# Kernel optimization log

Hardware: AMD Instinct MI355X
Metric: run time of the kernel (lower is better)

The kernel has to match this reference:

```python
import jax, jax.numpy as jnp
import numpy as np

TEMPERATURE = 0.07
EPS = 1e-8  # torch CosineSimilarity eps


def setup_inputs() -> dict:
    key = jax.random.key(0)
    k1, k2, k3 = jax.random.split(key, 3)
    N, D = 8192, 512
    features = jax.random.normal(k1, (N, D), dtype=jnp.float32)
    positive_mask = jax.random.randint(k2, (N, N), 0, 2, dtype=jnp.int32)
    negative_mask = jax.random.randint(k3, (N, N), 0, 2, dtype=jnp.int32)
    return {"features": features, "positive_mask": positive_mask, "negative_mask": negative_mask}


def reference(features, positive_mask, negative_mask):
    N = positive_mask.shape[0]
    self_contrast = 1.0 - jnp.eye(N, dtype=features.dtype)  # zero diagonal
    pos = positive_mask.astype(features.dtype) * self_contrast  # [N, N]
    neg = negative_mask.astype(features.dtype) * self_contrast  # [N, N]

    # cosine similarity via normalized matmul (same math as broadcasted CosineSimilarity)
    norm = jnp.maximum(jnp.linalg.norm(features, axis=1, keepdims=True), EPS)
    fn = features / norm  # [N, D]
    sim = jnp.matmul(fn, fn.T) / TEMPERATURE  # [N, N]

    logits_max = jax.lax.stop_gradient(jnp.max(sim, axis=1, keepdims=True))
    e = jnp.exp(sim - logits_max)  # [N, N]

    positives = e * pos
    log_neg_sum = jnp.log(jnp.sum(e * neg, axis=1, keepdims=True))  # [N, 1]
    log_prob = positives - log_neg_sum  # [N, N] (faithful to source: exp-masked, not log)

    cardinal = jnp.sum(pos, axis=1)
    cardinal = jnp.where(cardinal == 0, 1.0, cardinal)
    log_prob_sum = jnp.sum(log_prob * pos, axis=1)
    loss = -log_prob_sum / cardinal
    return jnp.mean(loss)
```

## Files before the change

### kernel.cpp

```cpp
#include <hip/hip_runtime.h>
#include <hip/hip_bf16.h>
#include <math.h>

#define NN 8192
#define DD 512
#define INV_T 14.285714285714286f

typedef __attribute__((ext_vector_type(8))) short s16x8;
typedef __attribute__((ext_vector_type(4))) float f32x4;
typedef __attribute__((ext_vector_type(4))) int   i32x4;
typedef __attribute__((ext_vector_type(4))) unsigned int u32x4;

__device__ __forceinline__ unsigned short f32_to_bf16(float f) {
  unsigned int u = __float_as_uint(f);
  u += 0x7FFFu + ((u >> 16) & 1u);
  return (unsigned short)(u >> 16);
}

__global__ __launch_bounds__(256) void normalize_kernel(const float* __restrict__ f,
                                                        unsigned short* __restrict__ fnb) {
  const int wave = threadIdx.x >> 6;
  const int lane = threadIdx.x & 63;
  const int row  = blockIdx.x * 4 + wave;
  const float* src = f + (size_t)row * DD + lane * 8;
  float4 v0 = *(const float4*)src;
  float4 v1 = *(const float4*)(src + 4);
  float ss = v0.x*v0.x + v0.y*v0.y + v0.z*v0.z + v0.w*v0.w
           + v1.x*v1.x + v1.y*v1.y + v1.z*v1.z + v1.w*v1.w;
  #pragma unroll
  for (int o = 32; o; o >>= 1) ss += __shfl_xor(ss, o);
  const float r = 1.0f / fmaxf(sqrtf(ss), 1e-8f);
  ushort4 a, b;
  a.x = f32_to_bf16(v0.x * r); a.y = f32_to_bf16(v0.y * r);
  a.z = f32_to_bf16(v0.z * r); a.w = f32_to_bf16(v0.w * r);
  b.x = f32_to_bf16(v1.x * r); b.y = f32_to_bf16(v1.y * r);
  b.z = f32_to_bf16(v1.z * r); b.w = f32_to_bf16(v1.w * r);
  unsigned short* dst = fnb + (size_t)row * DD + lane * 8;
  *(ushort4*)dst = a;
  *(ushort4*)(dst + 4) = b;
}

__global__ __launch_bounds__(256, 3) void fused_kernel(const unsigned short* __restrict__ fnb,
                                                       const int* __restrict__ posm,
                                                       const int* __restrict__ negm,
                                                       float* __restrict__ Spos,
                                                       float* __restrict__ Sneg,
                                                       float* __restrict__ Pcnt) {
  const int bid = blockIdx.x;
  int bi = (int)(64.5 - sqrt(64.5 * 64.5 - 2.0 * (double)bid));
  while (64 * bi - bi * (bi - 1) / 2 > bid) --bi;
  while (64 * (bi + 1) - (bi + 1) * bi / 2 <= bid) ++bi;
  const int bj = bi + (bid - (64 * bi - bi * (bi - 1) / 2));
  const int I = bi * 128;
  const int J = bj * 128;
  const bool offdiag = (bi != bj);

  const int tid  = threadIdx.x;
  const int wave = tid >> 6;
  const int lane = tid & 63;
  const int wm = wave >> 1;
  const int wn = wave & 1;
  const int q   = lane >> 4;
  const int c16 = lane & 15;

  __shared__ unsigned int bdir[2][128][4];
  __shared__ unsigned int btr [2][128][4];

  {
    const int tile = wave >> 1;
    const int msel = wave & 1;
    const int R0 = tile ? J : I;
    const int C0 = tile ? I : J;
    const int* mb = msel ? negm : posm;
    unsigned int (*dst)[4] = tile ? btr[msel] : bdir[msel];
    const int sub  = lane >> 5;
    const int col4 = (lane & 31) * 4;
    if (!(tile && !offdiag)) {
      for (int i = 0; i < 64; i += 4) {
        i32x4 v[4];
        #pragma unroll
        for (int u = 0; u < 4; ++u) {
          const int row = (i + u) * 2 + sub;
          v[u] = __builtin_nontemporal_load(
                   (const i32x4*)(mb + (size_t)(R0 + row) * NN + C0 + col4));
        }
        #pragma unroll
        for (int u = 0; u < 4; ++u) {
          const unsigned long long b0 = __ballot(v[u].x != 0);
          const unsigned long long b1 = __ballot(v[u].y != 0);
          const unsigned long long b2 = __ballot(v[u].z != 0);
          const unsigned long long b3 = __ballot(v[u].w != 0);
          if (lane < 2) {
            const int sh = lane * 32;
            u32x4 w;
            w.x = (unsigned int)(b0 >> sh);
            w.y = (unsigned int)(b1 >> sh);
            w.z = (unsigned int)(b2 >> sh);
            w.w = (unsigned int)(b3 >> sh);
            *(u32x4*)&dst[(i + u) * 2 + lane][0] = w;
          }
        }
      }
    }
  }

  f32x4 acc[4][4];
  const f32x4 z4 = {0.f, 0.f, 0.f, 0.f};
  #pragma unroll
  for (int mt = 0; mt < 4; ++mt)
    #pragma unroll
    for (int nt = 0; nt < 4; ++nt) acc[mt][nt] = z4;

  const unsigned short* aP[4];
  const unsigned short* bP[4];
  #pragma unroll
  for (int t = 0; t < 4; ++t) {
    aP[t] = fnb + (size_t)(I + wm * 64 + t * 16 + c16) * DD + q * 8;
    bP[t] = fnb + (size_t)(J + wn * 64 + t * 16 + c16) * DD + q * 8;
  }
  s16x8 aF[2][4], bF[2][4];
  #pragma unroll
  for (int t = 0; t < 4; ++t) {
    aF[0][t] = *(const s16x8*)aP[t];
    bF[0][t] = *(const s16x8*)bP[t];
  }
  #pragma unroll 2
  for (int kk = 0; kk < DD / 32; ++kk) {
    const int cur = kk & 1, nxt = cur ^ 1;
    if (kk < DD / 32 - 1) {
      const int off = (kk + 1) * 32;
      #pragma unroll
      for (int t = 0; t < 4; ++t) {
        aF[nxt][t] = *(const s16x8*)(aP[t] + off);
        bF[nxt][t] = *(const s16x8*)(bP[t] + off);
      }
    }
    #pragma unroll
    for (int mt = 0; mt < 4; ++mt)
      #pragma unroll
      for (int nt = 0; nt < 4; ++nt)
        acc[mt][nt] = __builtin_amdgcn_mfma_f32_16x16x32_bf16(aF[cur][mt], bF[cur][nt], acc[mt][nt], 0, 0, 0);
  }

  __syncthreads();

  const bool hasdiag = (bi == bj) && (wm == wn);

  u32x4 pT4[4], nT4[4];
  if (offdiag) {
    #pragma unroll
    for (int nt = 0; nt < 4; ++nt) {
      const int cl = wn * 64 + nt * 16 + c16;
      pT4[nt] = *(const u32x4*)&btr[0][cl][0];
      nT4[nt] = *(const u32x4*)&btr[1][cl][0];
    }
  }
  float tsp[4] = {0,0,0,0}, tsn[4] = {0,0,0,0};
  const int jword = c16 & 3;
  const int cshift = c16 >> 2;

  #pragma unroll
  for (int mt = 0; mt < 4; ++mt) {
    const int rl = wm * 64 + mt * 16 + q * 4;
    unsigned int pwv[4], nwv[4];
    #pragma unroll
    for (int r = 0; r < 4; ++r) {
      pwv[r] = bdir[0][rl + r][jword];
      nwv[r] = bdir[1][rl + r][jword];
    }
    float dsp[4] = {0,0,0,0}, dsn[4] = {0,0,0,0}, dpc[4] = {0,0,0,0};
    #pragma unroll
    for (int nt = 0; nt < 4; ++nt) {
      float e[4];
      #pragma unroll
      for (int r = 0; r < 4; ++r)
        e[r] = __expf(acc[mt][nt][r] * INV_T - INV_T);
      const int cbit = wn * 16 + nt * 4 + cshift;
      const int cl   = wn * 64 + nt * 16 + c16;
      #pragma unroll
      for (int r = 0; r < 4; ++r) {
        float pf = (float)((pwv[r] >> cbit) & 1u);
        float nf = (float)((nwv[r] >> cbit) & 1u);
        if (hasdiag && (rl + r == cl)) { pf = 0.f; nf = 0.f; }
        dsp[r] = fmaf(e[r], pf, dsp[r]);
        dsn[r] = fmaf(e[r], nf, dsn[r]);
        dpc[r] += pf;
      }
      if (offdiag) {
        const int tc = wm * 16 + mt * 4 + q;
        const unsigned int* pw = (const unsigned int*)&pT4[nt];
        const unsigned int* nw = (const unsigned int*)&nT4[nt];
        #pragma unroll
        for (int r = 0; r < 4; ++r) {
          tsp[nt] = fmaf(e[r], (float)((pw[r] >> tc) & 1u), tsp[nt]);
          tsn[nt] = fmaf(e[r], (float)((nw[r] >> tc) & 1u), tsn[nt]);
        }
      }
    }
    #pragma unroll
    for (int r = 0; r < 4; ++r) {
      float a = dsp[r], b = dsn[r], p = dpc[r];
      #pragma unroll
      for (int o = 1; o <= 8; o <<= 1) {
        a += __shfl_xor(a, o);
        b += __shfl_xor(b, o);
        p += __shfl_xor(p, o);
      }
      if (c16 == 0) {
        const int row = I + rl + r;
        atomicAdd(&Spos[row], a);
        atomicAdd(&Sneg[row], b);
        atomicAdd(&Pcnt[row], p);
      }
    }
  }

  if (offdiag) {
    #pragma unroll
    for (int nt = 0; nt < 4; ++nt) {
      float a = tsp[nt], b = tsn[nt];
      a += __shfl_xor(a, 16); a += __shfl_xor(a, 32);
      b += __shfl_xor(b, 16); b += __shfl_xor(b, 32);
      const int col = J + wn * 64 + nt * 16 + c16;
      if (q == 0) {
        atomicAdd(&Spos[col], a);
        atomicAdd(&Sneg[col], b);
      }
      if (q == 0 && wm == 0) {
        const unsigned int* pw = (const unsigned int*)&pT4[nt];
        const float pc = (float)(__popc(pw[0]) + __popc(pw[1]) + __popc(pw[2]) + __popc(pw[3]));
        atomicAdd(&Pcnt[col], pc);
      }
    }
  }
}

__global__ __launch_bounds__(256) void finalize_kernel(const float* __restrict__ Spos,
                                                       const float* __restrict__ Sneg,
                                                       const float* __restrict__ Pcnt,
                                                       float* __restrict__ out) {
  float local = 0.f;
  for (int i = threadIdx.x; i < NN; i += 256) {
    const float sp = Spos[i], sn = Sneg[i], pc = Pcnt[i];
    const float card = (pc == 0.f) ? 1.f : pc;
    local += (logf(sn) * pc - sp) / card;
  }
  #pragma unroll
  for (int o = 32; o; o >>= 1) local += __shfl_xor(local, o);
  __shared__ float red[4];
  if ((threadIdx.x & 63) == 0) red[threadIdx.x >> 6] = local;
  __syncthreads();
  if (threadIdx.x == 0)
    out[0] = (red[0] + red[1] + red[2] + red[3]) * (1.0f / (float)NN);
}

extern "C" void kernel_launch(void* const* d_in, const int* in_sizes, int n_in,
                              void* d_out, int out_size, void* d_ws, size_t ws_size,
                              hipStream_t stream) {
  const float* feat = (const float*)d_in[0];
  const int* posm   = (const int*)d_in[1];
  const int* negm   = (const int*)d_in[2];
  float* out = (float*)d_out;

  char* ws = (char*)d_ws;
  unsigned short* fnb = (unsigned short*)ws;
  float* Spos = (float*)(ws + (size_t)8 * 1024 * 1024);
  float* Sneg = Spos + NN;
  float* Pcnt = Sneg + NN;

  hipMemsetAsync(Spos, 0, 3 * NN * sizeof(float), stream);
  normalize_kernel<<<NN / 4, 256, 0, stream>>>(feat, fnb);
  fused_kernel<<<2080, 256, 0, stream>>>(fnb, posm, negm, Spos, Sneg, Pcnt);
  finalize_kernel<<<1, 256, 0, stream>>>(Spos, Sneg, Pcnt, out);
}
```

Before: 658.3 us.

## Interleave mask streaming with MFMA k-loop via software-pipelined loads

Mask loads and bit-packing no longer run as a separate phase before the matmul. They are split into 16 groups and issued three groups ahead inside the fully unrolled k-loop, so their HBM latency overlaps with the MFMA work. The bf16 fragment double buffer is dropped in favour of loading operands each iteration, and the occupancy hint drops from 3 to 2 waves per SIMD to make room for the mask register buffers. The risks are higher register pressure, lower occupancy and weaker latency hiding for the feature loads.

```diff
diff --git a/kernel.cpp b/kernel.cpp
--- a/kernel.cpp
+++ b/kernel.cpp
@@ -40,7 +40,7 @@
   *(ushort4*)(dst + 4) = b;
 }
 
-__global__ __launch_bounds__(256, 3) void fused_kernel(const unsigned short* __restrict__ fnb,
+__global__ __launch_bounds__(256, 2) void fused_kernel(const unsigned short* __restrict__ fnb,
                                                        const int* __restrict__ posm,
                                                        const int* __restrict__ negm,
                                                        float* __restrict__ Spos,
@@ -66,43 +66,47 @@
   __shared__ unsigned int bdir[2][128][4];
   __shared__ unsigned int btr [2][128][4];
 
-  {
-    const int tile = wave >> 1;
-    const int msel = wave & 1;
-    const int R0 = tile ? J : I;
-    const int C0 = tile ? I : J;
-    const int* mb = msel ? negm : posm;
-    unsigned int (*dst)[4] = tile ? btr[msel] : bdir[msel];
-    const int sub  = lane >> 5;
-    const int col4 = (lane & 31) * 4;
-    if (!(tile && !offdiag)) {
-      for (int i = 0; i < 64; i += 4) {
-        i32x4 v[4];
-        #pragma unroll
-        for (int u = 0; u < 4; ++u) {
-          const int row = (i + u) * 2 + sub;
-          v[u] = __builtin_nontemporal_load(
-                   (const i32x4*)(mb + (size_t)(R0 + row) * NN + C0 + col4));
-        }
-        #pragma unroll
-        for (int u = 0; u < 4; ++u) {
-          const unsigned long long b0 = __ballot(v[u].x != 0);
-          const unsigned long long b1 = __ballot(v[u].y != 0);
-          const unsigned long long b2 = __ballot(v[u].z != 0);
-          const unsigned long long b3 = __ballot(v[u].w != 0);
-          if (lane < 2) {
-            const int sh = lane * 32;
-            u32x4 w;
-            w.x = (unsigned int)(b0 >> sh);
-            w.y = (unsigned int)(b1 >> sh);
-            w.z = (unsigned int)(b2 >> sh);
-            w.w = (unsigned int)(b3 >> sh);
-            *(u32x4*)&dst[(i + u) * 2 + lane][0] = w;
-          }
-        }
-      }
-    }
-  }
+  const int tile = wave >> 1;
+  const int msel = wave & 1;
+  const int R0 = tile ? J : I;
+  const int C0 = tile ? I : J;
+  const int* mb = msel ? negm : posm;
+  unsigned int (*mdst)[4] = tile ? btr[msel] : bdir[msel];
+  const bool do_mask = !(tile && !offdiag);
+  const int sub  = lane >> 5;
+  const int col4 = (lane & 31) * 4;
+  const int* mrow = mb + (size_t)R0 * NN + C0 + col4;
+
+  i32x4 mg[4][4];
+
+  #define MISSUE(g)                                                           \
+    if (do_mask && (g) < 16) {                                                \
+      _Pragma("unroll")                                                       \
+      for (int u = 0; u < 4; ++u)                                             \
+        mg[(g) & 3][u] = __builtin_nontemporal_load(                          \
+            (const i32x4*)(mrow + (size_t)(8 * (g) + 2 * u + sub) * NN));     \
+    }
+
+  #define MDRAIN(g)                                                           \
+    if (do_mask) {                                                            \
+      _Pragma("unroll")                                                       \
+      for (int u = 0; u < 4; ++u) {                                           \
+        const i32x4 v = mg[(g) & 3][u];                                       \
+        const unsigned long long b0 = __ballot(v.x != 0);                     \
+        const unsigned long long b1 = __ballot(v.y != 0);                     \
+        const unsigned long long b2 = __ballot(v.z != 0);                     \
+        const unsigned long long b3 = __ballot(v.w != 0);                     \
+        if (lane < 2) {                                                       \
+          const int sh = lane * 32;                                           \
+          u32x4 w;                                                            \
+          w.x = (unsigned int)(b0 >> sh);                                     \
+          w.y = (unsigned int)(b1 >> sh);                                     \
+          w.z = (unsigned int)(b2 >> sh);                                     \
+          w.w = (unsigned int)(b3 >> sh);                                     \
+          *(u32x4*)&mdst[8 * (g) + 2 * u + lane][0] = w;                      \
+        }                                                                     \
+      }                                                                       \
+    }
 
   f32x4 acc[4][4];
   const f32x4 z4 = {0.f, 0.f, 0.f, 0.f};
@@ -118,28 +122,25 @@
     aP[t] = fnb + (size_t)(I + wm * 64 + t * 16 + c16) * DD + q * 8;
     bP[t] = fnb + (size_t)(J + wn * 64 + t * 16 + c16) * DD + q * 8;
   }
-  s16x8 aF[2][4], bF[2][4];
-  #pragma unroll
-  for (int t = 0; t < 4; ++t) {
-    aF[0][t] = *(const s16x8*)aP[t];
-    bF[0][t] = *(const s16x8*)bP[t];
-  }
-  #pragma unroll 2
-  for (int kk = 0; kk < DD / 32; ++kk) {
-    const int cur = kk & 1, nxt = cur ^ 1;
-    if (kk < DD / 32 - 1) {
-      const int off = (kk + 1) * 32;
-      #pragma unroll
-      for (int t = 0; t < 4; ++t) {
-        aF[nxt][t] = *(const s16x8*)(aP[t] + off);
-        bF[nxt][t] = *(const s16x8*)(bP[t] + off);
-      }
-    }
+
+  MISSUE(0) MISSUE(1) MISSUE(2)
+
+  #pragma unroll
+  for (int kk = 0; kk < 16; ++kk) {
+    MISSUE(kk + 3)
+    s16x8 aF[4], bF[4];
+    const int off = kk * 32;
+    #pragma unroll
+    for (int t = 0; t < 4; ++t) {
+      aF[t] = *(const s16x8*)(aP[t] + off);
+      bF[t] = *(const s16x8*)(bP[t] + off);
+    }
+    MDRAIN(kk)
     #pragma unroll
     for (int mt = 0; mt < 4; ++mt)
       #pragma unroll
       for (int nt = 0; nt < 4; ++nt)
-        acc[mt][nt] = __builtin_amdgcn_mfma_f32_16x16x32_bf16(aF[cur][mt], bF[cur][nt], acc[mt][nt], 0, 0, 0);
+        acc[mt][nt] = __builtin_amdgcn_mfma_f32_16x16x32_bf16(aF[mt], bF[nt], acc[mt][nt], 0, 0, 0);
   }
 
   __syncthreads();
```

New measurement: 642.1 us. -2.5%, faster.

## Load mask tiles directly into registers after GEMM instead of bit-packing via LDS

Applied to the files above, without the earlier changes.

Removes the prologue that loaded the positive and negative mask tiles, ballot-packed them into bitmasks and staged them in shared memory before the GEMM. The B-operand row mapping is permuted so each lane owns four consecutive columns. Each lane can then read its mask entries as int4 vectors straight from global memory in the epilogue, for both the direct and transposed tiles. This drops the LDS staging, the ballots and a block barrier. In exchange the mask loads are no longer overlapped with the MFMA loop, more registers are live, and the min-blocks launch hint is removed.

```diff
diff --git a/kernel.cpp b/kernel.cpp
--- a/kernel.cpp
+++ b/kernel.cpp
@@ -9,7 +9,6 @@
 typedef __attribute__((ext_vector_type(8))) short s16x8;
 typedef __attribute__((ext_vector_type(4))) float f32x4;
 typedef __attribute__((ext_vector_type(4))) int   i32x4;
-typedef __attribute__((ext_vector_type(4))) unsigned int u32x4;
 
 __device__ __forceinline__ unsigned short f32_to_bf16(float f) {
   unsigned int u = __float_as_uint(f);
@@ -40,12 +39,12 @@
   *(ushort4*)(dst + 4) = b;
 }
 
-__global__ __launch_bounds__(256, 3) void fused_kernel(const unsigned short* __restrict__ fnb,
-                                                       const int* __restrict__ posm,
-                                                       const int* __restrict__ negm,
-                                                       float* __restrict__ Spos,
-                                                       float* __restrict__ Sneg,
-                                                       float* __restrict__ Pcnt) {
+__global__ __launch_bounds__(256) void fused_kernel(const unsigned short* __restrict__ fnb,
+                                                    const int* __restrict__ posm,
+                                                    const int* __restrict__ negm,
+                                                    float* __restrict__ Spos,
+                                                    float* __restrict__ Sneg,
+                                                    float* __restrict__ Pcnt) {
   const int bid = blockIdx.x;
   int bi = (int)(64.5 - sqrt(64.5 * 64.5 - 2.0 * (double)bid));
   while (64 * bi - bi * (bi - 1) / 2 > bid) --bi;
@@ -63,47 +62,6 @@
   const int q   = lane >> 4;
   const int c16 = lane & 15;
 
-  __shared__ unsigned int bdir[2][128][4];
-  __shared__ unsigned int btr [2][128][4];
-
-  {
-    const int tile = wave >> 1;
-    const int msel = wave & 1;
-    const int R0 = tile ? J : I;
-    const int C0 = tile ? I : J;
-    const int* mb = msel ? negm : posm;
-    unsigned int (*dst)[4] = tile ? btr[msel] : bdir[msel];
-    const int sub  = lane >> 5;
-    const int col4 = (lane & 31) * 4;
-    if (!(tile && !offdiag)) {
-      for (int i = 0; i < 64; i += 4) {
-        i32x4 v[4];
-        #pragma unroll
-        for (int u = 0; u < 4; ++u) {
-          const int row = (i + u) * 2 + sub;
-          v[u] = __builtin_nontemporal_load(
-                   (const i32x4*)(mb + (size_t)(R0 + row) * NN + C0 + col4));
-        }
-        #pragma unroll
-        for (int u = 0; u < 4; ++u) {
-          const unsigned long long b0 = __ballot(v[u].x != 0);
-          const unsigned long long b1 = __ballot(v[u].y != 0);
-          const unsigned long long b2 = __ballot(v[u].z != 0);
-          const unsigned long long b3 = __ballot(v[u].w != 0);
-          if (lane < 2) {
-            const int sh = lane * 32;
-            u32x4 w;
-            w.x = (unsigned int)(b0 >> sh);
-            w.y = (unsigned int)(b1 >> sh);
-            w.z = (unsigned int)(b2 >> sh);
-            w.w = (unsigned int)(b3 >> sh);
-            *(u32x4*)&dst[(i + u) * 2 + lane][0] = w;
-          }
-        }
-      }
-    }
-  }
-
   f32x4 acc[4][4];
   const f32x4 z4 = {0.f, 0.f, 0.f, 0.f};
   #pragma unroll
@@ -116,7 +74,7 @@
   #pragma unroll
   for (int t = 0; t < 4; ++t) {
     aP[t] = fnb + (size_t)(I + wm * 64 + t * 16 + c16) * DD + q * 8;
-    bP[t] = fnb + (size_t)(J + wn * 64 + t * 16 + c16) * DD + q * 8;
+    bP[t] = fnb + (size_t)(J + wn * 64 + 4 * c16 + t) * DD + q * 8;
   }
   s16x8 aF[2][4], bF[2][4];
   #pragma unroll
@@ -142,59 +100,41 @@
         acc[mt][nt] = __builtin_amdgcn_mfma_f32_16x16x32_bf16(aF[cur][mt], bF[cur][nt], acc[mt][nt], 0, 0, 0);
   }
 
-  __syncthreads();
+  #pragma unroll
+  for (int mt = 0; mt < 4; ++mt)
+    #pragma unroll
+    for (int nt = 0; nt < 4; ++nt)
+      #pragma unroll
+      for (int r = 0; r < 4; ++r)
+        acc[mt][nt][r] = __expf(acc[mt][nt][r] * INV_T - INV_T);
 
   const bool hasdiag = (bi == bj) && (wm == wn);
-
-  u32x4 pT4[4], nT4[4];
-  if (offdiag) {
-    #pragma unroll
-    for (int nt = 0; nt < 4; ++nt) {
-      const int cl = wn * 64 + nt * 16 + c16;
-      pT4[nt] = *(const u32x4*)&btr[0][cl][0];
-      nT4[nt] = *(const u32x4*)&btr[1][cl][0];
-    }
-  }
-  float tsp[4] = {0,0,0,0}, tsn[4] = {0,0,0,0};
-  const int jword = c16 & 3;
-  const int cshift = c16 >> 2;
+  const int cb = wn * 64 + 4 * c16;
 
   #pragma unroll
   for (int mt = 0; mt < 4; ++mt) {
     const int rl = wm * 64 + mt * 16 + q * 4;
-    unsigned int pwv[4], nwv[4];
+    i32x4 pv[4], nv[4];
     #pragma unroll
     for (int r = 0; r < 4; ++r) {
-      pwv[r] = bdir[0][rl + r][jword];
-      nwv[r] = bdir[1][rl + r][jword];
-    }
-    float dsp[4] = {0,0,0,0}, dsn[4] = {0,0,0,0}, dpc[4] = {0,0,0,0};
-    #pragma unroll
-    for (int nt = 0; nt < 4; ++nt) {
-      float e[4];
-      #pragma unroll
-      for (int r = 0; r < 4; ++r)
-        e[r] = __expf(acc[mt][nt][r] * INV_T - INV_T);
-      const int cbit = wn * 16 + nt * 4 + cshift;
-      const int cl   = wn * 64 + nt * 16 + c16;
-      #pragma unroll
-      for (int r = 0; r < 4; ++r) {
-        float pf = (float)((pwv[r] >> cbit) & 1u);
-        float nf = (float)((nwv[r] >> cbit) & 1u);
-        if (hasdiag && (rl + r == cl)) { pf = 0.f; nf = 0.f; }
-        dsp[r] = fmaf(e[r], pf, dsp[r]);
-        dsn[r] = fmaf(e[r], nf, dsn[r]);
+      const size_t off = (size_t)(I + rl + r) * NN + J + cb;
+      pv[r] = __builtin_nontemporal_load((const i32x4*)(posm + off));
+      nv[r] = __builtin_nontemporal_load((const i32x4*)(negm + off));
+    }
+    float dsp[4], dsn[4], dpc[4];
+    #pragma unroll
+    for (int r = 0; r < 4; ++r) { dsp[r] = 0.f; dsn[r] = 0.f; dpc[r] = 0.f; }
+    #pragma unroll
+    for (int r = 0; r < 4; ++r) {
+      #pragma unroll
+      for (int nt = 0; nt < 4; ++nt) {
+        float pf = (float)pv[r][nt];
+        float nf = (float)nv[r][nt];
+        if (hasdiag && (rl + r == cb + nt)) { pf = 0.f; nf = 0.f; }
+        const float e = acc[mt][nt][r];
+        dsp[r] = fmaf(e, pf, dsp[r]);
+        dsn[r] = fmaf(e, nf, dsn[r]);
         dpc[r] += pf;
-      }
-      if (offdiag) {
-        const int tc = wm * 16 + mt * 4 + q;
-        const unsigned int* pw = (const unsigned int*)&pT4[nt];
-        const unsigned int* nw = (const unsigned int*)&nT4[nt];
-        #pragma unroll
-        for (int r = 0; r < 4; ++r) {
-          tsp[nt] = fmaf(e[r], (float)((pw[r] >> tc) & 1u), tsp[nt]);
-          tsn[nt] = fmaf(e[r], (float)((nw[r] >> tc) & 1u), tsn[nt]);
-        }
       }
     }
     #pragma unroll
@@ -218,18 +158,34 @@
   if (offdiag) {
     #pragma unroll
     for (int nt = 0; nt < 4; ++nt) {
-      float a = tsp[nt], b = tsn[nt];
-      a += __shfl_xor(a, 16); a += __shfl_xor(a, 32);
-      b += __shfl_xor(b, 16); b += __shfl_xor(b, 32);
-      const int col = J + wn * 64 + nt * 16 + c16;
+      const int trow = J + cb + nt;
+      i32x4 pv[4], nv[4];
+      #pragma unroll
+      for (int mt = 0; mt < 4; ++mt) {
+        const size_t off = (size_t)trow * NN + I + wm * 64 + mt * 16 + q * 4;
+        pv[mt] = __builtin_nontemporal_load((const i32x4*)(posm + off));
+        nv[mt] = __builtin_nontemporal_load((const i32x4*)(negm + off));
+      }
+      float ts = 0.f, tn = 0.f, tp = 0.f;
+      #pragma unroll
+      for (int mt = 0; mt < 4; ++mt) {
+        #pragma unroll
+        for (int r = 0; r < 4; ++r) {
+          const float pf = (float)pv[mt][r];
+          const float nf = (float)nv[mt][r];
+          const float e  = acc[mt][nt][r];
+          ts = fmaf(e, pf, ts);
+          tn = fmaf(e, nf, tn);
+          tp += pf;
+        }
+      }
+      ts += __shfl_xor(ts, 16); ts += __shfl_xor(ts, 32);
+      tn += __shfl_xor(tn, 16); tn += __shfl_xor(tn, 32);
+      tp += __shfl_xor(tp, 16); tp += __shfl_xor(tp, 32);
       if (q == 0) {
-        atomicAdd(&Spos[col], a);
-        atomicAdd(&Sneg[col], b);
-      }
-      if (q == 0 && wm == 0) {
-        const unsigned int* pw = (const unsigned int*)&pT4[nt];
-        const float pc = (float)(__popc(pw[0]) + __popc(pw[1]) + __popc(pw[2]) + __popc(pw[3]));
-        atomicAdd(&Pcnt[col], pc);
+        atomicAdd(&Spos[trow], ts);
+        atomicAdd(&Sneg[trow], tn);
+        atomicAdd(&Pcnt[trow], tp);
       }
     }
   }
```

After: 668.6 us. Within noise of the previous version (+1.6%).
